# Optimization experiments

Measured on AMD Instinct MI355X. Metric: run time of the kernel, lower is better.

Reference implementation:

```python
import jax, jax.numpy as jnp
import numpy as np

CLIP = 50.0
EPS = 1e-8


def _attn_jacobian_agg(q, k, v, scale):
    """Aggregate attention Jacobian dO/dq summed over queries, plus attention outputs.

    q: (B, Q, d); k, v: (B, S, d).
    Per-query Jacobian: J_q = scale * sum_j p_j v_j (k_j - kbar)^T, kbar = sum_i p_i k_i.
    Returns (agg_jac: (B, d, d), outputs: (B, Q, d)).
    """
    scores = jnp.einsum('bqd,bsd->bqs', q, k) * scale
    p = jax.nn.softmax(scores, axis=-1)
    out = jnp.einsum('bqs,bsd->bqd', p, v)           # attention outputs O
    kbar = jnp.einsum('bqs,bsd->bqd', p, k)          # expected key per query
    # sum_j p_j v_j k_j^T  -> (B, Q, d, d)
    pvk = jnp.einsum('bqs,bsd,bse->bqde', p, v, k)
    jac = scale * (pvk - out[..., :, None] * kbar[..., None, :])
    return jac.sum(axis=1), out


def setup_inputs() -> dict:
    key = jax.random.key(0)
    ks = jax.random.split(key, 5)
    B, Q, S, M, D = 256, 16, 512, 8, 128
    return {
        'queries': jax.random.normal(ks[0], (B, Q, D), dtype=jnp.float32),
        'keys':    jax.random.normal(ks[1], (B, S, D), dtype=jnp.float32),
        'values':  jax.random.normal(ks[2], (B, S, D), dtype=jnp.float32),
        'k_cg':    jax.random.normal(ks[3], (B, M, D), dtype=jnp.float32),
        'v_cg':    jax.random.normal(ks[4], (B, M, D), dtype=jnp.float32),
    }


def reference(queries, keys, values, k_cg, v_cg):
    B, Q, d = queries.shape
    scale = d ** -0.5

    dense_jac, dense_out = _attn_jacobian_agg(queries, keys, values, scale)
    cg_jac, cg_out = _attn_jacobian_agg(queries, k_cg, v_cg, scale)

    # jacobian_clip_value = 50.0 (config default)
    dense_jac = jnp.clip(dense_jac, -CLIP, CLIP)
    cg_jac = jnp.clip(cg_jac, -CLIP, CLIP)

    df = dense_jac.reshape(B, -1)
    cf = cg_jac.reshape(B, -1)
    dn = jnp.linalg.norm(df, axis=-1)
    cn = jnp.linalg.norm(cf, axis=-1)
    cosine_sim = (df * cf).sum(axis=-1) / (dn * cn + EPS)
    force_direction_loss = 1.0 - cosine_sim

    # consistency: per-query output MSE, averaged over queries, scaled by 1/d_head
    out_diff = dense_out - cg_out
    per_query_mse = (out_diff ** 2).sum(axis=-1)          # (B, Q)
    consistency_loss = per_query_mse.sum(axis=-1) / Q / d  # (B,)

    # v4 loss: L = w_dir * L_force_cos + w_cons * L_consistency (defaults 1.0, 1.0)
    total = 1.0 * force_direction_loss + 1.0 * consistency_loss
    return total.mean()  # reduction='mean'
```

## Files before the change

### kernel.cpp

```cpp
#include <hip/hip_runtime.h>
#include <math.h>


namespace {
constexpr int Bn = 256, Qn = 16, Sn = 512, Mn = 8, Dn = 128;
constexpr int NT = 512;
constexpr float SCALE = 0.08838834764831845f;
constexpr float CLIPV = 50.0f;

constexpr int QS    = 0;
constexpr int PB    = 4352;
constexpr int WOFF  = 20992;
constexpr int ARENA = 23040;
constexpr int KT    = ARENA;
constexpr int VT    = ARENA + 18432;
constexpr int VTW   = ARENA + 27648;
constexpr int SCF   = ARENA;
constexpr int CGS   = 59904;
constexpr int PCG   = 60416;
constexpr int WC    = 61696;
constexpr int RED   = 61728;
constexpr int LDSZ  = 61856;

typedef __attribute__((ext_vector_type(8))) short bf16x8;
typedef __attribute__((ext_vector_type(4))) float f32x4;
#define MFMA16(a, b, c) __builtin_amdgcn_mfma_f32_16x16x32_bf16((a), (b), (c), 0, 0, 0)

__device__ inline unsigned int pack2t(float a, float b) {
  return __builtin_amdgcn_perm(__builtin_bit_cast(unsigned int, b),
                               __builtin_bit_cast(unsigned int, a), 0x07060302u);
}
__device__ inline unsigned short f2bf(float x) {
  unsigned int u = __builtin_bit_cast(unsigned int, x);
  u += 0x7fffu + ((u >> 16) & 1u);
  return (unsigned short)(u >> 16);
}
__device__ inline float bf2f(unsigned short h) {
  unsigned int u = ((unsigned int)h) << 16;
  return __builtin_bit_cast(float, u);
}
union Frag {
  bf16x8 v;
  unsigned int u[4];
  unsigned short h[8];
};

__global__ void zero_ws_kernel(float4* ws) {
  ws[threadIdx.x] = make_float4(0.f, 0.f, 0.f, 0.f);
}

__global__ void finalize_kernel(const float* __restrict__ ws, float* __restrict__ out) {
  __shared__ float sr[256];
  int i = threadIdx.x;
  float dt = ws[i * 4 + 0], n1 = ws[i * 4 + 1], n2 = ws[i * 4 + 2], cs = ws[i * 4 + 3];
  float cosv = dt / (sqrtf(n1) * sqrtf(n2) + 1e-8f);
  sr[i] = (1.0f - cosv) + cs * (1.0f / (float)(Qn * Dn));
  __syncthreads();
  for (int off = 128; off; off >>= 1) {
    if (i < off) sr[i] += sr[i + off];
    __syncthreads();
  }
  if (i == 0) out[0] = sr[0] * (1.0f / (float)Bn);
}

__global__ __launch_bounds__(NT, 4) void fm_kernel(
    const float* __restrict__ Qg, const float* __restrict__ Kg,
    const float* __restrict__ Vg, const float* __restrict__ Kcg,
    const float* __restrict__ Vcg, float* __restrict__ ws) {
  __shared__ __align__(16) char L[LDSZ];
  const int bid = blockIdx.x, b = bid >> 1, h = bid & 1;
  const int t = threadIdx.x, lane = t & 63, wv = t >> 6;
  const int quad = lane >> 4, l16 = lane & 15;

  const float* Qb = Qg + (size_t)b * Qn * Dn;
  const float* Kb = Kg + (size_t)b * Sn * Dn;
  const float* Vb = Vg + (size_t)b * Sn * Dn;
  const float* Kc = Kcg + (size_t)b * Mn * Dn;
  const float* Vc = Vcg + (size_t)b * Mn * Dn;

  const int dK = t & 127, gK = t >> 7;
  const int dV = t & 63, gV = t >> 6;
  float kpf[2][8], vpf[8];

  auto load_tiles = [&](int st) {
#pragma unroll
    for (int o = 0; o < 2; ++o) {
      int s0 = st * 64 + (gK + 4 * o) * 8;
#pragma unroll
      for (int i = 0; i < 8; ++i) kpf[o][i] = Kb[(size_t)(s0 + i) * Dn + dK];
    }
    int s1 = st * 64 + gV * 8;
#pragma unroll
    for (int i = 0; i < 8; ++i) vpf[i] = Vb[(size_t)(s1 + i) * Dn + h * 64 + dV];
  };
  auto store_tiles = [&](int st) {
#pragma unroll
    for (int o = 0; o < 2; ++o) {
      unsigned int u0 = pack2t(kpf[o][0], kpf[o][1]), u1 = pack2t(kpf[o][2], kpf[o][3]);
      unsigned int u2 = pack2t(kpf[o][4], kpf[o][5]), u3 = pack2t(kpf[o][6], kpf[o][7]);
      *(uint4*)(L + KT + dK * 144 + (gK + 4 * o) * 16) = make_uint4(u0, u1, u2, u3);
    }
    int s1 = st * 64 + gV * 8;
    float wv8[8];
#pragma unroll
    for (int i = 0; i < 8; ++i) wv8[i] = *(const float*)(L + WOFF + (s1 + i) * 4);
    unsigned int v0 = pack2t(vpf[0], vpf[1]), v1 = pack2t(vpf[2], vpf[3]);
    unsigned int v2 = pack2t(vpf[4], vpf[5]), v3 = pack2t(vpf[6], vpf[7]);
    *(uint4*)(L + VT + dV * 144 + gV * 16) = make_uint4(v0, v1, v2, v3);
    unsigned int w0 = pack2t(wv8[0] * vpf[0], wv8[1] * vpf[1]);
    unsigned int w1 = pack2t(wv8[2] * vpf[2], wv8[3] * vpf[3]);
    unsigned int w2 = pack2t(wv8[4] * vpf[4], wv8[5] * vpf[5]);
    unsigned int w3 = pack2t(wv8[6] * vpf[6], wv8[7] * vpf[7]);
    *(uint4*)(L + VTW + dV * 144 + gV * 16) = make_uint4(w0, w1, w2, w3);
  };

  {
    int row = t >> 5, c4 = t & 31;
    float4 qv = ((const float4*)Qb)[t];
    unsigned int p0 = pack2t(qv.x * SCALE, qv.y * SCALE);
    unsigned int p1 = pack2t(qv.z * SCALE, qv.w * SCALE);
    *(unsigned long long*)(L + QS + row * 272 + c4 * 8) =
        (unsigned long long)p0 | ((unsigned long long)p1 << 32);
  }
  load_tiles(0);
  __syncthreads();

  {
    bf16x8 aq[4];
#pragma unroll
    for (int kk = 0; kk < 4; ++kk)
      aq[kk] = *(const bf16x8*)(L + QS + l16 * 272 + kk * 64 + quad * 16);
    for (int j = 0; j < 4; ++j) {
      int srow = 64 * wv + 16 * j + l16;
      const float* kp = Kb + (size_t)srow * Dn + quad * 8;
      f32x4 acc = {0.f, 0.f, 0.f, 0.f};
#pragma unroll
      for (int kk = 0; kk < 4; ++kk) {
        float4 lo = *(const float4*)(kp + kk * 32);
        float4 hi = *(const float4*)(kp + kk * 32 + 4);
        Frag f;
        f.u[0] = pack2t(lo.x, lo.y);
        f.u[1] = pack2t(lo.z, lo.w);
        f.u[2] = pack2t(hi.x, hi.y);
        f.u[3] = pack2t(hi.z, hi.w);
        acc = MFMA16(aq[kk], f.v, acc);
      }
      int s = 64 * wv + 16 * j + l16;
#pragma unroll
      for (int r = 0; r < 4; ++r)
        *(float*)(L + SCF + (quad * 4 + r) * 2064 + s * 4) = acc[r];
    }
  }
  __syncthreads();

#pragma unroll
  for (int rr = 0; rr < 2; ++rr) {
    int q = wv * 2 + rr;
    const float* srow = (const float*)(L + SCF + q * 2064);
    float x[8];
    float m = -1e30f;
#pragma unroll
    for (int i = 0; i < 8; ++i) { x[i] = srow[lane * 8 + i]; m = fmaxf(m, x[i]); }
#pragma unroll
    for (int o = 32; o; o >>= 1) m = fmaxf(m, __shfl_xor(m, o));
    float ssum = 0.f;
#pragma unroll
    for (int i = 0; i < 8; ++i) { x[i] = __expf(x[i] - m); ssum += x[i]; }
#pragma unroll
    for (int o = 32; o; o >>= 1) ssum += __shfl_xor(ssum, o);
    float inv = 1.f / ssum;
    Frag g;
#pragma unroll
    for (int i = 0; i < 8; ++i) g.h[i] = f2bf(x[i] * inv);
    *(bf16x8*)(L + PB + q * 1040 + lane * 16) = g.v;
  }
  __syncthreads();
  {
    float wsv = 0.f;
#pragma unroll
    for (int q = 0; q < Qn; ++q)
      wsv += bf2f(*(const unsigned short*)(L + PB + q * 1040 + t * 2));
    *(float*)(L + WOFF + t * 4) = wsv;
  }
  __syncthreads();

  const int rp = wv & 1, ch = wv >> 1;
  f32x4 C00 = {0.f,0.f,0.f,0.f}, C01 = {0.f,0.f,0.f,0.f};
  f32x4 C10 = {0.f,0.f,0.f,0.f}, C11 = {0.f,0.f,0.f,0.f};
  f32x4 outacc = {0.f,0.f,0.f,0.f}, kbacc = {0.f,0.f,0.f,0.f};

  auto ckstep = [&](int colByte, f32x4& c00, f32x4& c01, f32x4& c10, f32x4& c11) {
    bf16x8 A0 = *(const bf16x8*)(L + VTW + (rp * 32 + l16) * 144 + colByte + quad * 16);
    bf16x8 A1 = *(const bf16x8*)(L + VTW + (rp * 32 + 16 + l16) * 144 + colByte + quad * 16);
    bf16x8 B0 = *(const bf16x8*)(L + KT + (ch * 32 + l16) * 144 + colByte + quad * 16);
    bf16x8 B1 = *(const bf16x8*)(L + KT + (ch * 32 + 16 + l16) * 144 + colByte + quad * 16);
    c00 = MFMA16(A0, B0, c00);
    c01 = MFMA16(A0, B1, c01);
    c10 = MFMA16(A1, B0, c10);
    c11 = MFMA16(A1, B1, c11);
  };

  for (int st = 0; st < 8; ++st) {
    if (st) __syncthreads();
    store_tiles(st);
    __syncthreads();
    if (st < 7) load_tiles(st + 1);
#pragma unroll
    for (int z = 0; z < 2; ++z) {
      int colByte = z * 64;
      bf16x8 pA = *(const bf16x8*)(L + PB + l16 * 1040 + st * 128 + z * 64 + quad * 16);
      bf16x8 bK = *(const bf16x8*)(L + KT + (wv * 16 + l16) * 144 + colByte + quad * 16);
      kbacc = MFMA16(pA, bK, kbacc);
      if (wv < 4) {
        bf16x8 bV = *(const bf16x8*)(L + VT + (wv * 16 + l16) * 144 + colByte + quad * 16);
        outacc = MFMA16(pA, bV, outacc);
      }
      ckstep(colByte, C00, C01, C10, C11);
    }
  }
  __syncthreads();

  if (wv < 4) {
#pragma unroll
    for (int r = 0; r < 4; ++r)
      *(unsigned short*)(L + VTW + (wv * 16 + l16) * 144 + (quad * 4 + r) * 2) = f2bf(-outacc[r]);
  }
#pragma unroll
  for (int r = 0; r < 4; ++r)
    *(unsigned short*)(L + KT + (wv * 16 + l16) * 144 + (quad * 4 + r) * 2) = f2bf(kbacc[r]);
  if (t < 256) {
    *(uint4*)(L + KT + (t >> 1) * 144 + 32 + (t & 1) * 16) = make_uint4(0, 0, 0, 0);
  } else if (t < 384) {
    int i = t - 256;
    *(uint4*)(L + VTW + (i >> 1) * 144 + 32 + (i & 1) * 16) = make_uint4(0, 0, 0, 0);
  }
  __syncthreads();
  ckstep(0, C00, C01, C10, C11);
#pragma unroll
  for (int r = 0; r < 4; ++r) {
    C00[r] = fminf(fmaxf(SCALE * C00[r], -CLIPV), CLIPV);
    C01[r] = fminf(fmaxf(SCALE * C01[r], -CLIPV), CLIPV);
    C10[r] = fminf(fmaxf(SCALE * C10[r], -CLIPV), CLIPV);
    C11[r] = fminf(fmaxf(SCALE * C11[r], -CLIPV), CLIPV);
  }
  __syncthreads();

  if (wv == 0) {
    f32x4 acc = {0.f, 0.f, 0.f, 0.f};
    const float* kp = Kc + (size_t)(l16 & 7) * Dn + quad * 8;
#pragma unroll
    for (int kk = 0; kk < 4; ++kk) {
      bf16x8 a = *(const bf16x8*)(L + QS + l16 * 272 + kk * 64 + quad * 16);
      float4 lo = *(const float4*)(kp + kk * 32);
      float4 hi = *(const float4*)(kp + kk * 32 + 4);
      Frag f;
      f.u[0] = pack2t(lo.x, lo.y);
      f.u[1] = pack2t(lo.z, lo.w);
      f.u[2] = pack2t(hi.x, hi.y);
      f.u[3] = pack2t(hi.z, hi.w);
      acc = MFMA16(a, f.v, acc);
    }
    if (l16 < 8) {
#pragma unroll
      for (int r = 0; r < 4; ++r)
        *(float*)(L + CGS + (quad * 4 + r) * 32 + l16 * 4) = acc[r];
    }
  }
  __syncthreads();
  if (t < 16) {
    float xs[8];
    float m = -1e30f;
#pragma unroll
    for (int s = 0; s < 8; ++s) { xs[s] = *(const float*)(L + CGS + t * 32 + s * 4); m = fmaxf(m, xs[s]); }
    float ssum = 0.f;
#pragma unroll
    for (int s = 0; s < 8; ++s) { xs[s] = __expf(xs[s] - m); ssum += xs[s]; }
    float inv = 1.f / ssum;
#pragma unroll
    for (int s = 0; s < 4; ++s)
      *(unsigned int*)(L + PCG + t * 80 + s * 4) = pack2t(xs[2 * s] * inv, xs[2 * s + 1] * inv);
#pragma unroll
    for (int p = 4; p < 16; ++p) *(unsigned int*)(L + PCG + t * 80 + p * 4) = 0u;
  }
  __syncthreads();
  if (t < 8) {
    float s = 0.f;
#pragma unroll
    for (int q = 0; q < Qn; ++q) s += bf2f(*(const unsigned short*)(L + PCG + q * 80 + t * 2));
    *(float*)(L + WC + t * 4) = s;
  }
  __syncthreads();
  if (t < 128) {
    float kv[8];
#pragma unroll
    for (int i = 0; i < 8; ++i) kv[i] = Kc[(size_t)i * Dn + t];
    *(uint4*)(L + KT + t * 144) = make_uint4(pack2t(kv[0], kv[1]), pack2t(kv[2], kv[3]),
                                             pack2t(kv[4], kv[5]), pack2t(kv[6], kv[7]));
    *(uint4*)(L + KT + t * 144 + 16) = make_uint4(0, 0, 0, 0);
    *(uint4*)(L + KT + t * 144 + 32) = make_uint4(0, 0, 0, 0);
    *(uint4*)(L + KT + t * 144 + 48) = make_uint4(0, 0, 0, 0);
  } else if (t < 192) {
    int d = t - 128;
    float vv2[8];
#pragma unroll
    for (int i = 0; i < 8; ++i) vv2[i] = Vc[(size_t)i * Dn + h * 64 + d];
    *(uint4*)(L + VT + d * 144) = make_uint4(pack2t(vv2[0], vv2[1]), pack2t(vv2[2], vv2[3]),
                                             pack2t(vv2[4], vv2[5]), pack2t(vv2[6], vv2[7]));
    *(uint4*)(L + VT + d * 144 + 16) = make_uint4(0, 0, 0, 0);
    *(uint4*)(L + VT + d * 144 + 32) = make_uint4(0, 0, 0, 0);
    *(uint4*)(L + VT + d * 144 + 48) = make_uint4(0, 0, 0, 0);
  } else if (t < 256) {
    int d = t - 192;
    float vv2[8], wcv[8];
#pragma unroll
    for (int i = 0; i < 8; ++i) {
      vv2[i] = Vc[(size_t)i * Dn + h * 64 + d];
      wcv[i] = *(const float*)(L + WC + i * 4);
    }
    *(uint4*)(L + VTW + d * 144) =
        make_uint4(pack2t(wcv[0] * vv2[0], wcv[1] * vv2[1]), pack2t(wcv[2] * vv2[2], wcv[3] * vv2[3]),
                   pack2t(wcv[4] * vv2[4], wcv[5] * vv2[5]), pack2t(wcv[6] * vv2[6], wcv[7] * vv2[7]));
    *(uint4*)(L + VTW + d * 144 + 16) = make_uint4(0, 0, 0, 0);
    *(uint4*)(L + VTW + d * 144 + 32) = make_uint4(0, 0, 0, 0);
    *(uint4*)(L + VTW + d * 144 + 48) = make_uint4(0, 0, 0, 0);
  }
  __syncthreads();
  f32x4 outc = {0.f,0.f,0.f,0.f}, kbc = {0.f,0.f,0.f,0.f};
  f32x4 D00 = {0.f,0.f,0.f,0.f}, D01 = {0.f,0.f,0.f,0.f};
  f32x4 D10 = {0.f,0.f,0.f,0.f}, D11 = {0.f,0.f,0.f,0.f};
  {
    bf16x8 pA = *(const bf16x8*)(L + PCG + l16 * 80 + quad * 16);
    bf16x8 bK = *(const bf16x8*)(L + KT + (wv * 16 + l16) * 144 + quad * 16);
    kbc = MFMA16(pA, bK, kbc);
    if (wv < 4) {
      bf16x8 bV = *(const bf16x8*)(L + VT + (wv * 16 + l16) * 144 + quad * 16);
      outc = MFMA16(pA, bV, outc);
    }
    ckstep(0, D00, D01, D10, D11);
  }
  __syncthreads();
  if (wv < 4) {
#pragma unroll
    for (int r = 0; r < 4; ++r)
      *(unsigned short*)(L + VTW + (wv * 16 + l16) * 144 + (quad * 4 + r) * 2) = f2bf(-outc[r]);
  }
#pragma unroll
  for (int r = 0; r < 4; ++r)
    *(unsigned short*)(L + KT + (wv * 16 + l16) * 144 + (quad * 4 + r) * 2) = f2bf(kbc[r]);
  __syncthreads();
  ckstep(0, D00, D01, D10, D11);
#pragma unroll
  for (int r = 0; r < 4; ++r) {
    D00[r] = fminf(fmaxf(SCALE * D00[r], -CLIPV), CLIPV);
    D01[r] = fminf(fmaxf(SCALE * D01[r], -CLIPV), CLIPV);
    D10[r] = fminf(fmaxf(SCALE * D10[r], -CLIPV), CLIPV);
    D11[r] = fminf(fmaxf(SCALE * D11[r], -CLIPV), CLIPV);
  }

  float dot = 0.f, nd2 = 0.f, nc2 = 0.f, cons = 0.f;
#pragma unroll
  for (int r = 0; r < 4; ++r) {
    dot += C00[r] * D00[r] + C01[r] * D01[r] + C10[r] * D10[r] + C11[r] * D11[r];
    nd2 += C00[r] * C00[r] + C01[r] * C01[r] + C10[r] * C10[r] + C11[r] * C11[r];
    nc2 += D00[r] * D00[r] + D01[r] * D01[r] + D10[r] * D10[r] + D11[r] * D11[r];
  }
  if (wv < 4) {
#pragma unroll
    for (int r = 0; r < 4; ++r) {
      float df = outacc[r] - outc[r];
      cons += df * df;
    }
  }
#pragma unroll
  for (int o = 32; o; o >>= 1) {
    dot += __shfl_xor(dot, o);
    nd2 += __shfl_xor(nd2, o);
    nc2 += __shfl_xor(nc2, o);
    cons += __shfl_xor(cons, o);
  }
  if (lane == 0) {
    float* red = (float*)(L + RED);
    red[wv * 4 + 0] = dot;
    red[wv * 4 + 1] = nd2;
    red[wv * 4 + 2] = nc2;
    red[wv * 4 + 3] = cons;
  }
  __syncthreads();
  if (t == 0) {
    const float* red = (const float*)(L + RED);
    float d_ = 0.f, n1 = 0.f, n2 = 0.f, cs = 0.f;
#pragma unroll
    for (int w = 0; w < 8; ++w) {
      d_ += red[w * 4 + 0];
      n1 += red[w * 4 + 1];
      n2 += red[w * 4 + 2];
      cs += red[w * 4 + 3];
    }
    atomicAdd(ws + b * 4 + 0, d_);
    atomicAdd(ws + b * 4 + 1, n1);
    atomicAdd(ws + b * 4 + 2, n2);
    atomicAdd(ws + b * 4 + 3, cs);
  }
}
}

extern "C" void kernel_launch(void* const* d_in, const int* in_sizes, int n_in,
                              void* d_out, int out_size, void* d_ws, size_t ws_size,
                              hipStream_t stream) {
  const float* q = (const float*)d_in[0];
  const float* k = (const float*)d_in[1];
  const float* v = (const float*)d_in[2];
  const float* kc = (const float*)d_in[3];
  const float* vc = (const float*)d_in[4];
  float* out = (float*)d_out;
  float* ws = (float*)d_ws;
  zero_ws_kernel<<<1, 256, 0, stream>>>((float4*)ws);
  fm_kernel<<<2 * Bn, NT, 0, stream>>>(q, k, v, kc, vc, ws);
  finalize_kernel<<<1, 256, 0, stream>>>(ws, out);
}
```

Measured before the change: 169.0 us.

## Split scores/softmax into separate per-batch kernel, removing duplicate work across halves

Before, each of the two blocks per batch recomputed the full Q·K scores, softmax and column weights. Now a separate scores_kernel does this once per batch, with register-resident softmax reductions, and writes probabilities, weights and the coarse-grained probabilities to the workspace. jac_kernel reads these back, and its block index is remapped so that both halves of a batch run close together for L2 reuse. The zero kernel is folded into scores_kernel. The cost is an extra launch and a global-memory round trip for the probability matrix, and K is read one more time.

```diff
diff --git a/kernel.cpp b/kernel.cpp
--- a/kernel.cpp
+++ b/kernel.cpp
@@ -8,19 +8,10 @@
 constexpr float SCALE = 0.08838834764831845f;
 constexpr float CLIPV = 50.0f;
 
-constexpr int QS    = 0;
-constexpr int PB    = 4352;
-constexpr int WOFF  = 20992;
-constexpr int ARENA = 23040;
-constexpr int KT    = ARENA;
-constexpr int VT    = ARENA + 18432;
-constexpr int VTW   = ARENA + 27648;
-constexpr int SCF   = ARENA;
-constexpr int CGS   = 59904;
-constexpr int PCG   = 60416;
-constexpr int WC    = 61696;
-constexpr int RED   = 61728;
-constexpr int LDSZ  = 61856;
+constexpr int W_OFF_F = 1048576;
+constexpr int PCG_OFF_B = 4718592;
+constexpr int WC_OFF_F = 1196032;
+constexpr int PART_OFF_F = 1198080;
 
 typedef __attribute__((ext_vector_type(8))) short bf16x8;
 typedef __attribute__((ext_vector_type(4))) float f32x4;
@@ -45,212 +36,43 @@
   unsigned short h[8];
 };
 
-__global__ void zero_ws_kernel(float4* ws) {
-  ws[threadIdx.x] = make_float4(0.f, 0.f, 0.f, 0.f);
-}
-
-__global__ void finalize_kernel(const float* __restrict__ ws, float* __restrict__ out) {
-  __shared__ float sr[256];
-  int i = threadIdx.x;
-  float dt = ws[i * 4 + 0], n1 = ws[i * 4 + 1], n2 = ws[i * 4 + 2], cs = ws[i * 4 + 3];
-  float cosv = dt / (sqrtf(n1) * sqrtf(n2) + 1e-8f);
-  sr[i] = (1.0f - cosv) + cs * (1.0f / (float)(Qn * Dn));
-  __syncthreads();
-  for (int off = 128; off; off >>= 1) {
-    if (i < off) sr[i] += sr[i + off];
-    __syncthreads();
-  }
-  if (i == 0) out[0] = sr[0] * (1.0f / (float)Bn);
-}
-
-__global__ __launch_bounds__(NT, 4) void fm_kernel(
+constexpr int A_QS = 0, A_PB = 4352, A_RDM = 20992, A_RDS = 21504,
+              A_CGS = 22016, A_CGP = 22528, A_LDSZ = 22784;
+
+__global__ __launch_bounds__(NT) void scores_kernel(
     const float* __restrict__ Qg, const float* __restrict__ Kg,
-    const float* __restrict__ Vg, const float* __restrict__ Kcg,
-    const float* __restrict__ Vcg, float* __restrict__ ws) {
-  __shared__ __align__(16) char L[LDSZ];
-  const int bid = blockIdx.x, b = bid >> 1, h = bid & 1;
-  const int t = threadIdx.x, lane = t & 63, wv = t >> 6;
-  const int quad = lane >> 4, l16 = lane & 15;
-
+    const float* __restrict__ Kcg, float* __restrict__ ws) {
+  __shared__ __align__(16) char L[A_LDSZ];
+  const int b = blockIdx.x, t = threadIdx.x;
+  const int lane = t & 63, wv = t >> 6, quad = lane >> 4, l16 = lane & 15;
   const float* Qb = Qg + (size_t)b * Qn * Dn;
   const float* Kb = Kg + (size_t)b * Sn * Dn;
-  const float* Vb = Vg + (size_t)b * Sn * Dn;
   const float* Kc = Kcg + (size_t)b * Mn * Dn;
-  const float* Vc = Vcg + (size_t)b * Mn * Dn;
-
-  const int dK = t & 127, gK = t >> 7;
-  const int dV = t & 63, gV = t >> 6;
-  float kpf[2][8], vpf[8];
-
-  auto load_tiles = [&](int st) {
-#pragma unroll
-    for (int o = 0; o < 2; ++o) {
-      int s0 = st * 64 + (gK + 4 * o) * 8;
-#pragma unroll
-      for (int i = 0; i < 8; ++i) kpf[o][i] = Kb[(size_t)(s0 + i) * Dn + dK];
-    }
-    int s1 = st * 64 + gV * 8;
-#pragma unroll
-    for (int i = 0; i < 8; ++i) vpf[i] = Vb[(size_t)(s1 + i) * Dn + h * 64 + dV];
-  };
-  auto store_tiles = [&](int st) {
-#pragma unroll
-    for (int o = 0; o < 2; ++o) {
-      unsigned int u0 = pack2t(kpf[o][0], kpf[o][1]), u1 = pack2t(kpf[o][2], kpf[o][3]);
-      unsigned int u2 = pack2t(kpf[o][4], kpf[o][5]), u3 = pack2t(kpf[o][6], kpf[o][7]);
-      *(uint4*)(L + KT + dK * 144 + (gK + 4 * o) * 16) = make_uint4(u0, u1, u2, u3);
-    }
-    int s1 = st * 64 + gV * 8;
-    float wv8[8];
-#pragma unroll
-    for (int i = 0; i < 8; ++i) wv8[i] = *(const float*)(L + WOFF + (s1 + i) * 4);
-    unsigned int v0 = pack2t(vpf[0], vpf[1]), v1 = pack2t(vpf[2], vpf[3]);
-    unsigned int v2 = pack2t(vpf[4], vpf[5]), v3 = pack2t(vpf[6], vpf[7]);
-    *(uint4*)(L + VT + dV * 144 + gV * 16) = make_uint4(v0, v1, v2, v3);
-    unsigned int w0 = pack2t(wv8[0] * vpf[0], wv8[1] * vpf[1]);
-    unsigned int w1 = pack2t(wv8[2] * vpf[2], wv8[3] * vpf[3]);
-    unsigned int w2 = pack2t(wv8[4] * vpf[4], wv8[5] * vpf[5]);
-    unsigned int w3 = pack2t(wv8[6] * vpf[6], wv8[7] * vpf[7]);
-    *(uint4*)(L + VTW + dV * 144 + gV * 16) = make_uint4(w0, w1, w2, w3);
-  };
+
+  if (t == 0)
+    *(float4*)(ws + PART_OFF_F + b * 4) = make_float4(0.f, 0.f, 0.f, 0.f);
 
   {
     int row = t >> 5, c4 = t & 31;
     float4 qv = ((const float4*)Qb)[t];
     unsigned int p0 = pack2t(qv.x * SCALE, qv.y * SCALE);
     unsigned int p1 = pack2t(qv.z * SCALE, qv.w * SCALE);
-    *(unsigned long long*)(L + QS + row * 272 + c4 * 8) =
+    *(unsigned long long*)(L + A_QS + row * 272 + c4 * 8) =
         (unsigned long long)p0 | ((unsigned long long)p1 << 32);
   }
-  load_tiles(0);
-  __syncthreads();
-
-  {
-    bf16x8 aq[4];
-#pragma unroll
-    for (int kk = 0; kk < 4; ++kk)
-      aq[kk] = *(const bf16x8*)(L + QS + l16 * 272 + kk * 64 + quad * 16);
-    for (int j = 0; j < 4; ++j) {
-      int srow = 64 * wv + 16 * j + l16;
-      const float* kp = Kb + (size_t)srow * Dn + quad * 8;
-      f32x4 acc = {0.f, 0.f, 0.f, 0.f};
-#pragma unroll
-      for (int kk = 0; kk < 4; ++kk) {
-        float4 lo = *(const float4*)(kp + kk * 32);
-        float4 hi = *(const float4*)(kp + kk * 32 + 4);
-        Frag f;
-        f.u[0] = pack2t(lo.x, lo.y);
-        f.u[1] = pack2t(lo.z, lo.w);
-        f.u[2] = pack2t(hi.x, hi.y);
-        f.u[3] = pack2t(hi.z, hi.w);
-        acc = MFMA16(aq[kk], f.v, acc);
-      }
-      int s = 64 * wv + 16 * j + l16;
-#pragma unroll
-      for (int r = 0; r < 4; ++r)
-        *(float*)(L + SCF + (quad * 4 + r) * 2064 + s * 4) = acc[r];
-    }
-  }
-  __syncthreads();
-
-#pragma unroll
-  for (int rr = 0; rr < 2; ++rr) {
-    int q = wv * 2 + rr;
-    const float* srow = (const float*)(L + SCF + q * 2064);
-    float x[8];
-    float m = -1e30f;
-#pragma unroll
-    for (int i = 0; i < 8; ++i) { x[i] = srow[lane * 8 + i]; m = fmaxf(m, x[i]); }
-#pragma unroll
-    for (int o = 32; o; o >>= 1) m = fmaxf(m, __shfl_xor(m, o));
-    float ssum = 0.f;
-#pragma unroll
-    for (int i = 0; i < 8; ++i) { x[i] = __expf(x[i] - m); ssum += x[i]; }
-#pragma unroll
-    for (int o = 32; o; o >>= 1) ssum += __shfl_xor(ssum, o);
-    float inv = 1.f / ssum;
-    Frag g;
-#pragma unroll
-    for (int i = 0; i < 8; ++i) g.h[i] = f2bf(x[i] * inv);
-    *(bf16x8*)(L + PB + q * 1040 + lane * 16) = g.v;
-  }
-  __syncthreads();
-  {
-    float wsv = 0.f;
-#pragma unroll
-    for (int q = 0; q < Qn; ++q)
-      wsv += bf2f(*(const unsigned short*)(L + PB + q * 1040 + t * 2));
-    *(float*)(L + WOFF + t * 4) = wsv;
-  }
-  __syncthreads();
-
-  const int rp = wv & 1, ch = wv >> 1;
-  f32x4 C00 = {0.f,0.f,0.f,0.f}, C01 = {0.f,0.f,0.f,0.f};
-  f32x4 C10 = {0.f,0.f,0.f,0.f}, C11 = {0.f,0.f,0.f,0.f};
-  f32x4 outacc = {0.f,0.f,0.f,0.f}, kbacc = {0.f,0.f,0.f,0.f};
-
-  auto ckstep = [&](int colByte, f32x4& c00, f32x4& c01, f32x4& c10, f32x4& c11) {
-    bf16x8 A0 = *(const bf16x8*)(L + VTW + (rp * 32 + l16) * 144 + colByte + quad * 16);
-    bf16x8 A1 = *(const bf16x8*)(L + VTW + (rp * 32 + 16 + l16) * 144 + colByte + quad * 16);
-    bf16x8 B0 = *(const bf16x8*)(L + KT + (ch * 32 + l16) * 144 + colByte + quad * 16);
-    bf16x8 B1 = *(const bf16x8*)(L + KT + (ch * 32 + 16 + l16) * 144 + colByte + quad * 16);
-    c00 = MFMA16(A0, B0, c00);
-    c01 = MFMA16(A0, B1, c01);
-    c10 = MFMA16(A1, B0, c10);
-    c11 = MFMA16(A1, B1, c11);
-  };
-
-  for (int st = 0; st < 8; ++st) {
-    if (st) __syncthreads();
-    store_tiles(st);
-    __syncthreads();
-    if (st < 7) load_tiles(st + 1);
-#pragma unroll
-    for (int z = 0; z < 2; ++z) {
-      int colByte = z * 64;
-      bf16x8 pA = *(const bf16x8*)(L + PB + l16 * 1040 + st * 128 + z * 64 + quad * 16);
-      bf16x8 bK = *(const bf16x8*)(L + KT + (wv * 16 + l16) * 144 + colByte + quad * 16);
-      kbacc = MFMA16(pA, bK, kbacc);
-      if (wv < 4) {
-        bf16x8 bV = *(const bf16x8*)(L + VT + (wv * 16 + l16) * 144 + colByte + quad * 16);
-        outacc = MFMA16(pA, bV, outacc);
-      }
-      ckstep(colByte, C00, C01, C10, C11);
-    }
-  }
-  __syncthreads();
-
-  if (wv < 4) {
-#pragma unroll
-    for (int r = 0; r < 4; ++r)
-      *(unsigned short*)(L + VTW + (wv * 16 + l16) * 144 + (quad * 4 + r) * 2) = f2bf(-outacc[r]);
-  }
-#pragma unroll
-  for (int r = 0; r < 4; ++r)
-    *(unsigned short*)(L + KT + (wv * 16 + l16) * 144 + (quad * 4 + r) * 2) = f2bf(kbacc[r]);
-  if (t < 256) {
-    *(uint4*)(L + KT + (t >> 1) * 144 + 32 + (t & 1) * 16) = make_uint4(0, 0, 0, 0);
-  } else if (t < 384) {
-    int i = t - 256;
-    *(uint4*)(L + VTW + (i >> 1) * 144 + 32 + (i & 1) * 16) = make_uint4(0, 0, 0, 0);
-  }
-  __syncthreads();
-  ckstep(0, C00, C01, C10, C11);
-#pragma unroll
-  for (int r = 0; r < 4; ++r) {
-    C00[r] = fminf(fmaxf(SCALE * C00[r], -CLIPV), CLIPV);
-    C01[r] = fminf(fmaxf(SCALE * C01[r], -CLIPV), CLIPV);
-    C10[r] = fminf(fmaxf(SCALE * C10[r], -CLIPV), CLIPV);
-    C11[r] = fminf(fmaxf(SCALE * C11[r], -CLIPV), CLIPV);
-  }
-  __syncthreads();
-
-  if (wv == 0) {
-    f32x4 acc = {0.f, 0.f, 0.f, 0.f};
-    const float* kp = Kc + (size_t)(l16 & 7) * Dn + quad * 8;
+  __syncthreads();
+
+  bf16x8 aq[4];
+#pragma unroll
+  for (int kk = 0; kk < 4; ++kk)
+    aq[kk] = *(const bf16x8*)(L + A_QS + l16 * 272 + kk * 64 + quad * 16);
+  f32x4 acc[4];
+#pragma unroll
+  for (int j = 0; j < 4; ++j) {
+    const float* kp = Kb + (size_t)(64 * wv + 16 * j + l16) * Dn + quad * 8;
+    f32x4 a = {0.f, 0.f, 0.f, 0.f};
 #pragma unroll
     for (int kk = 0; kk < 4; ++kk) {
-      bf16x8 a = *(const bf16x8*)(L + QS + l16 * 272 + kk * 64 + quad * 16);
       float4 lo = *(const float4*)(kp + kk * 32);
       float4 hi = *(const float4*)(kp + kk * 32 + 4);
       Frag f;
@@ -258,82 +80,307 @@
       f.u[1] = pack2t(lo.z, lo.w);
       f.u[2] = pack2t(hi.x, hi.y);
       f.u[3] = pack2t(hi.z, hi.w);
-      acc = MFMA16(a, f.v, acc);
-    }
-    if (l16 < 8) {
+      a = MFMA16(aq[kk], f.v, a);
+    }
+    acc[j] = a;
+  }
+  {
+    float pm[4];
+#pragma unroll
+    for (int r = 0; r < 4; ++r)
+      pm[r] = fmaxf(fmaxf(acc[0][r], acc[1][r]), fmaxf(acc[2][r], acc[3][r]));
+#pragma unroll
+    for (int o = 1; o < 16; o <<= 1)
+#pragma unroll
+      for (int r = 0; r < 4; ++r) pm[r] = fmaxf(pm[r], __shfl_xor(pm[r], o));
+    if (l16 == 0)
+#pragma unroll
+      for (int r = 0; r < 4; ++r) *(float*)(L + A_RDM + (quad * 4 + r) * 32 + wv * 4) = pm[r];
+  }
+  __syncthreads();
+  float gm[4];
+#pragma unroll
+  for (int r = 0; r < 4; ++r) {
+    const float* p = (const float*)(L + A_RDM + (quad * 4 + r) * 32);
+    float m = p[0];
+#pragma unroll
+    for (int w = 1; w < 8; ++w) m = fmaxf(m, p[w]);
+    gm[r] = m;
+  }
+  float e[4][4];
+  {
+    float ps[4] = {0.f, 0.f, 0.f, 0.f};
+#pragma unroll
+    for (int j = 0; j < 4; ++j)
+#pragma unroll
+      for (int r = 0; r < 4; ++r) {
+        e[j][r] = __expf(acc[j][r] - gm[r]);
+        ps[r] += e[j][r];
+      }
+#pragma unroll
+    for (int o = 1; o < 16; o <<= 1)
+#pragma unroll
+      for (int r = 0; r < 4; ++r) ps[r] += __shfl_xor(ps[r], o);
+    if (l16 == 0)
+#pragma unroll
+      for (int r = 0; r < 4; ++r) *(float*)(L + A_RDS + (quad * 4 + r) * 32 + wv * 4) = ps[r];
+  }
+  __syncthreads();
+  float inv[4];
+#pragma unroll
+  for (int r = 0; r < 4; ++r) {
+    const float* p = (const float*)(L + A_RDS + (quad * 4 + r) * 32);
+    float s = 0.f;
+#pragma unroll
+    for (int w = 0; w < 8; ++w) s += p[w];
+    inv[r] = 1.f / s;
+  }
+#pragma unroll
+  for (int j = 0; j < 4; ++j)
+#pragma unroll
+    for (int r = 0; r < 4; ++r)
+      *(unsigned short*)(L + A_PB + (quad * 4 + r) * 1040 + (64 * wv + 16 * j + l16) * 2) =
+          f2bf(e[j][r] * inv[r]);
+  __syncthreads();
+  {
+    float wsum = 0.f;
+#pragma unroll
+    for (int q = 0; q < Qn; ++q)
+      wsum += bf2f(*(const unsigned short*)(L + A_PB + q * 1040 + t * 2));
+    ws[W_OFF_F + b * 512 + t] = wsum;
+  }
+#pragma unroll
+  for (int i = 0; i < 2; ++i) {
+    int idx = t + i * 512, q = idx >> 6, c = idx & 63;
+    *(uint4*)((char*)ws + (size_t)b * 16384 + q * 1024 + c * 16) =
+        *(const uint4*)(L + A_PB + q * 1040 + c * 16);
+  }
+  if (wv == 0) {
+    const float* kp = Kc + (size_t)(l16 & 7) * Dn + quad * 8;
+    f32x4 a = {0.f, 0.f, 0.f, 0.f};
+#pragma unroll
+    for (int kk = 0; kk < 4; ++kk) {
+      float4 lo = *(const float4*)(kp + kk * 32);
+      float4 hi = *(const float4*)(kp + kk * 32 + 4);
+      Frag f;
+      f.u[0] = pack2t(lo.x, lo.y);
+      f.u[1] = pack2t(lo.z, lo.w);
+      f.u[2] = pack2t(hi.x, hi.y);
+      f.u[3] = pack2t(hi.z, hi.w);
+      a = MFMA16(aq[kk], f.v, a);
+    }
+    if (l16 < 8)
 #pragma unroll
       for (int r = 0; r < 4; ++r)
-        *(float*)(L + CGS + (quad * 4 + r) * 32 + l16 * 4) = acc[r];
-    }
+        *(float*)(L + A_CGS + (quad * 4 + r) * 32 + l16 * 4) = a[r];
   }
   __syncthreads();
   if (t < 16) {
     float xs[8];
     float m = -1e30f;
 #pragma unroll
-    for (int s = 0; s < 8; ++s) { xs[s] = *(const float*)(L + CGS + t * 32 + s * 4); m = fmaxf(m, xs[s]); }
+    for (int s = 0; s < 8; ++s) {
+      xs[s] = *(const float*)(L + A_CGS + t * 32 + s * 4);
+      m = fmaxf(m, xs[s]);
+    }
     float ssum = 0.f;
 #pragma unroll
-    for (int s = 0; s < 8; ++s) { xs[s] = __expf(xs[s] - m); ssum += xs[s]; }
-    float inv = 1.f / ssum;
-#pragma unroll
-    for (int s = 0; s < 4; ++s)
-      *(unsigned int*)(L + PCG + t * 80 + s * 4) = pack2t(xs[2 * s] * inv, xs[2 * s + 1] * inv);
-#pragma unroll
-    for (int p = 4; p < 16; ++p) *(unsigned int*)(L + PCG + t * 80 + p * 4) = 0u;
+    for (int s = 0; s < 8; ++s) {
+      xs[s] = __expf(xs[s] - m);
+      ssum += xs[s];
+    }
+    float iv = 1.f / ssum;
+    uint4 pk = make_uint4(pack2t(xs[0] * iv, xs[1] * iv), pack2t(xs[2] * iv, xs[3] * iv),
+                          pack2t(xs[4] * iv, xs[5] * iv), pack2t(xs[6] * iv, xs[7] * iv));
+    *(uint4*)(L + A_CGP + t * 16) = pk;
+    *(uint4*)((char*)ws + PCG_OFF_B + b * 256 + t * 16) = pk;
   }
   __syncthreads();
   if (t < 8) {
     float s = 0.f;
 #pragma unroll
-    for (int q = 0; q < Qn; ++q) s += bf2f(*(const unsigned short*)(L + PCG + q * 80 + t * 2));
-    *(float*)(L + WC + t * 4) = s;
-  }
-  __syncthreads();
+    for (int q = 0; q < Qn; ++q)
+      s += bf2f(*(const unsigned short*)(L + A_CGP + q * 16 + t * 2));
+    ws[WC_OFF_F + b * 8 + t] = s;
+  }
+}
+
+constexpr int B_PB = 0, B_WOFF = 16640, B_KT = 18688, B_VT = 37120, B_VTW = 46336,
+              B_PCG = 55552, B_WC = 56832, B_RED = 56864, B_LDSZ = 56992;
+
+__global__ __launch_bounds__(NT, 4) void jac_kernel(
+    const float* __restrict__ Kg, const float* __restrict__ Vg,
+    const float* __restrict__ Kcg, const float* __restrict__ Vcg,
+    float* __restrict__ ws) {
+  __shared__ __align__(16) char L[B_LDSZ];
+  const int g = blockIdx.x;
+  const int h = (g >> 3) & 1;
+  const int b = (g & 7) | ((g >> 4) << 3);
+  const int t = threadIdx.x, lane = t & 63, wv = t >> 6;
+  const int quad = lane >> 4, l16 = lane & 15;
+
+  const float* Kb = Kg + (size_t)b * Sn * Dn;
+  const float* Vb = Vg + (size_t)b * Sn * Dn;
+  const float* Kc = Kcg + (size_t)b * Mn * Dn;
+  const float* Vc = Vcg + (size_t)b * Mn * Dn;
+
+  const int dK = t & 127, gK = t >> 7;
+  const int dV = t & 63, gV = t >> 6;
+  float kpf[2][8], vpf[8];
+
+  auto load_tiles = [&](int st) {
+#pragma unroll
+    for (int o = 0; o < 2; ++o) {
+      int s0 = st * 64 + (gK + 4 * o) * 8;
+#pragma unroll
+      for (int i = 0; i < 8; ++i) kpf[o][i] = Kb[(size_t)(s0 + i) * Dn + dK];
+    }
+    int s1 = st * 64 + gV * 8;
+#pragma unroll
+    for (int i = 0; i < 8; ++i) vpf[i] = Vb[(size_t)(s1 + i) * Dn + h * 64 + dV];
+  };
+  auto store_tiles = [&](int st) {
+#pragma unroll
+    for (int o = 0; o < 2; ++o) {
+      unsigned int u0 = pack2t(kpf[o][0], kpf[o][1]), u1 = pack2t(kpf[o][2], kpf[o][3]);
+      unsigned int u2 = pack2t(kpf[o][4], kpf[o][5]), u3 = pack2t(kpf[o][6], kpf[o][7]);
+      *(uint4*)(L + B_KT + dK * 144 + (gK + 4 * o) * 16) = make_uint4(u0, u1, u2, u3);
+    }
+    int s1 = st * 64 + gV * 8;
+    float w8[8];
+#pragma unroll
+    for (int i = 0; i < 8; ++i) w8[i] = *(const float*)(L + B_WOFF + (s1 + i) * 4);
+    *(uint4*)(L + B_VT + dV * 144 + gV * 16) =
+        make_uint4(pack2t(vpf[0], vpf[1]), pack2t(vpf[2], vpf[3]),
+                   pack2t(vpf[4], vpf[5]), pack2t(vpf[6], vpf[7]));
+    *(uint4*)(L + B_VTW + dV * 144 + gV * 16) =
+        make_uint4(pack2t(w8[0] * vpf[0], w8[1] * vpf[1]), pack2t(w8[2] * vpf[2], w8[3] * vpf[3]),
+                   pack2t(w8[4] * vpf[4], w8[5] * vpf[5]), pack2t(w8[6] * vpf[6], w8[7] * vpf[7]));
+  };
+
+#pragma unroll
+  for (int i = 0; i < 2; ++i) {
+    int idx = t + i * 512, q = idx >> 6, c = idx & 63;
+    *(uint4*)(L + B_PB + q * 1040 + c * 16) =
+        *(const uint4*)((const char*)ws + (size_t)b * 16384 + q * 1024 + c * 16);
+  }
+  *(float*)(L + B_WOFF + t * 4) = ws[W_OFF_F + b * 512 + t];
+  if (t < 16) {
+    uint4 pv = *(const uint4*)((const char*)ws + PCG_OFF_B + b * 256 + t * 16);
+    *(uint4*)(L + B_PCG + t * 80) = pv;
+    *(uint4*)(L + B_PCG + t * 80 + 16) = make_uint4(0, 0, 0, 0);
+    *(uint4*)(L + B_PCG + t * 80 + 32) = make_uint4(0, 0, 0, 0);
+    *(uint4*)(L + B_PCG + t * 80 + 48) = make_uint4(0, 0, 0, 0);
+  }
+  if (t < 8) *(float*)(L + B_WC + t * 4) = ws[WC_OFF_F + b * 8 + t];
+  load_tiles(0);
+  __syncthreads();
+
+  const int rp = wv & 1, ch = wv >> 1;
+  f32x4 C00 = {0.f,0.f,0.f,0.f}, C01 = {0.f,0.f,0.f,0.f};
+  f32x4 C10 = {0.f,0.f,0.f,0.f}, C11 = {0.f,0.f,0.f,0.f};
+  f32x4 outacc = {0.f,0.f,0.f,0.f}, kbacc = {0.f,0.f,0.f,0.f};
+
+  auto ckstep = [&](int colByte, f32x4& c00, f32x4& c01, f32x4& c10, f32x4& c11) {
+    bf16x8 A0 = *(const bf16x8*)(L + B_VTW + (rp * 32 + l16) * 144 + colByte + quad * 16);
+    bf16x8 A1 = *(const bf16x8*)(L + B_VTW + (rp * 32 + 16 + l16) * 144 + colByte + quad * 16);
+    bf16x8 B0 = *(const bf16x8*)(L + B_KT + (ch * 32 + l16) * 144 + colByte + quad * 16);
+    bf16x8 B1 = *(const bf16x8*)(L + B_KT + (ch * 32 + 16 + l16) * 144 + colByte + quad * 16);
+    c00 = MFMA16(A0, B0, c00);
+    c01 = MFMA16(A0, B1, c01);
+    c10 = MFMA16(A1, B0, c10);
+    c11 = MFMA16(A1, B1, c11);
+  };
+
+  for (int st = 0; st < 8; ++st) {
+    if (st) __syncthreads();
+    store_tiles(st);
+    __syncthreads();
+    if (st < 7) load_tiles(st + 1);
+#pragma unroll
+    for (int z = 0; z < 2; ++z) {
+      int colByte = z * 64;
+      bf16x8 pA = *(const bf16x8*)(L + B_PB + l16 * 1040 + st * 128 + z * 64 + quad * 16);
+      bf16x8 bK = *(const bf16x8*)(L + B_KT + (wv * 16 + l16) * 144 + colByte + quad * 16);
+      kbacc = MFMA16(pA, bK, kbacc);
+      if (wv < 4) {
+        bf16x8 bV = *(const bf16x8*)(L + B_VT + (wv * 16 + l16) * 144 + colByte + quad * 16);
+        outacc = MFMA16(pA, bV, outacc);
+      }
+      ckstep(colByte, C00, C01, C10, C11);
+    }
+  }
+  __syncthreads();
+
+  if (wv < 4) {
+#pragma unroll
+    for (int r = 0; r < 4; ++r)
+      *(unsigned short*)(L + B_VTW + (wv * 16 + l16) * 144 + (quad * 4 + r) * 2) = f2bf(-outacc[r]);
+  }
+#pragma unroll
+  for (int r = 0; r < 4; ++r)
+    *(unsigned short*)(L + B_KT + (wv * 16 + l16) * 144 + (quad * 4 + r) * 2) = f2bf(kbacc[r]);
+  if (t < 256) {
+    *(uint4*)(L + B_KT + (t >> 1) * 144 + 32 + (t & 1) * 16) = make_uint4(0, 0, 0, 0);
+  } else if (t < 384) {
+    int i = t - 256;
+    *(uint4*)(L + B_VTW + (i >> 1) * 144 + 32 + (i & 1) * 16) = make_uint4(0, 0, 0, 0);
+  }
+  __syncthreads();
+  ckstep(0, C00, C01, C10, C11);
+#pragma unroll
+  for (int r = 0; r < 4; ++r) {
+    C00[r] = fminf(fmaxf(SCALE * C00[r], -CLIPV), CLIPV);
+    C01[r] = fminf(fmaxf(SCALE * C01[r], -CLIPV), CLIPV);
+    C10[r] = fminf(fmaxf(SCALE * C10[r], -CLIPV), CLIPV);
+    C11[r] = fminf(fmaxf(SCALE * C11[r], -CLIPV), CLIPV);
+  }
+  __syncthreads();
+
   if (t < 128) {
     float kv[8];
 #pragma unroll
     for (int i = 0; i < 8; ++i) kv[i] = Kc[(size_t)i * Dn + t];
-    *(uint4*)(L + KT + t * 144) = make_uint4(pack2t(kv[0], kv[1]), pack2t(kv[2], kv[3]),
-                                             pack2t(kv[4], kv[5]), pack2t(kv[6], kv[7]));
-    *(uint4*)(L + KT + t * 144 + 16) = make_uint4(0, 0, 0, 0);
-    *(uint4*)(L + KT + t * 144 + 32) = make_uint4(0, 0, 0, 0);
-    *(uint4*)(L + KT + t * 144 + 48) = make_uint4(0, 0, 0, 0);
+    *(uint4*)(L + B_KT + t * 144) = make_uint4(pack2t(kv[0], kv[1]), pack2t(kv[2], kv[3]),
+                                               pack2t(kv[4], kv[5]), pack2t(kv[6], kv[7]));
+    *(uint4*)(L + B_KT + t * 144 + 16) = make_uint4(0, 0, 0, 0);
+    *(uint4*)(L + B_KT + t * 144 + 32) = make_uint4(0, 0, 0, 0);
+    *(uint4*)(L + B_KT + t * 144 + 48) = make_uint4(0, 0, 0, 0);
   } else if (t < 192) {
     int d = t - 128;
-    float vv2[8];
-#pragma unroll
-    for (int i = 0; i < 8; ++i) vv2[i] = Vc[(size_t)i * Dn + h * 64 + d];
-    *(uint4*)(L + VT + d * 144) = make_uint4(pack2t(vv2[0], vv2[1]), pack2t(vv2[2], vv2[3]),
-                                             pack2t(vv2[4], vv2[5]), pack2t(vv2[6], vv2[7]));
-    *(uint4*)(L + VT + d * 144 + 16) = make_uint4(0, 0, 0, 0);
-    *(uint4*)(L + VT + d * 144 + 32) = make_uint4(0, 0, 0, 0);
-    *(uint4*)(L + VT + d * 144 + 48) = make_uint4(0, 0, 0, 0);
+    float v2[8];
+#pragma unroll
+    for (int i = 0; i < 8; ++i) v2[i] = Vc[(size_t)i * Dn + h * 64 + d];
+    *(uint4*)(L + B_VT + d * 144) = make_uint4(pack2t(v2[0], v2[1]), pack2t(v2[2], v2[3]),
+                                               pack2t(v2[4], v2[5]), pack2t(v2[6], v2[7]));
+    *(uint4*)(L + B_VT + d * 144 + 16) = make_uint4(0, 0, 0, 0);
+    *(uint4*)(L + B_VT + d * 144 + 32) = make_uint4(0, 0, 0, 0);
+    *(uint4*)(L + B_VT + d * 144 + 48) = make_uint4(0, 0, 0, 0);
   } else if (t < 256) {
     int d = t - 192;
-    float vv2[8], wcv[8];
+    float v2[8], wc[8];
 #pragma unroll
     for (int i = 0; i < 8; ++i) {
-      vv2[i] = Vc[(size_t)i * Dn + h * 64 + d];
-      wcv[i] = *(const float*)(L + WC + i * 4);
-    }
-    *(uint4*)(L + VTW + d * 144) =
-        make_uint4(pack2t(wcv[0] * vv2[0], wcv[1] * vv2[1]), pack2t(wcv[2] * vv2[2], wcv[3] * vv2[3]),
-                   pack2t(wcv[4] * vv2[4], wcv[5] * vv2[5]), pack2t(wcv[6] * vv2[6], wcv[7] * vv2[7]));
-    *(uint4*)(L + VTW + d * 144 + 16) = make_uint4(0, 0, 0, 0);
-    *(uint4*)(L + VTW + d * 144 + 32) = make_uint4(0, 0, 0, 0);
-    *(uint4*)(L + VTW + d * 144 + 48) = make_uint4(0, 0, 0, 0);
+      v2[i] = Vc[(size_t)i * Dn + h * 64 + d];
+      wc[i] = *(const float*)(L + B_WC + i * 4);
+    }
+    *(uint4*)(L + B_VTW + d * 144) =
+        make_uint4(pack2t(wc[0] * v2[0], wc[1] * v2[1]), pack2t(wc[2] * v2[2], wc[3] * v2[3]),
+                   pack2t(wc[4] * v2[4], wc[5] * v2[5]), pack2t(wc[6] * v2[6], wc[7] * v2[7]));
+    *(uint4*)(L + B_VTW + d * 144 + 16) = make_uint4(0, 0, 0, 0);
+    *(uint4*)(L + B_VTW + d * 144 + 32) = make_uint4(0, 0, 0, 0);
+    *(uint4*)(L + B_VTW + d * 144 + 48) = make_uint4(0, 0, 0, 0);
   }
   __syncthreads();
   f32x4 outc = {0.f,0.f,0.f,0.f}, kbc = {0.f,0.f,0.f,0.f};
   f32x4 D00 = {0.f,0.f,0.f,0.f}, D01 = {0.f,0.f,0.f,0.f};
   f32x4 D10 = {0.f,0.f,0.f,0.f}, D11 = {0.f,0.f,0.f,0.f};
   {
-    bf16x8 pA = *(const bf16x8*)(L + PCG + l16 * 80 + quad * 16);
-    bf16x8 bK = *(const bf16x8*)(L + KT + (wv * 16 + l16) * 144 + quad * 16);
+    bf16x8 pA = *(const bf16x8*)(L + B_PCG + l16 * 80 + quad * 16);
+    bf16x8 bK = *(const bf16x8*)(L + B_KT + (wv * 16 + l16) * 144 + quad * 16);
     kbc = MFMA16(pA, bK, kbc);
     if (wv < 4) {
-      bf16x8 bV = *(const bf16x8*)(L + VT + (wv * 16 + l16) * 144 + quad * 16);
+      bf16x8 bV = *(const bf16x8*)(L + B_VT + (wv * 16 + l16) * 144 + quad * 16);
       outc = MFMA16(pA, bV, outc);
     }
     ckstep(0, D00, D01, D10, D11);
@@ -342,11 +389,11 @@
   if (wv < 4) {
 #pragma unroll
     for (int r = 0; r < 4; ++r)
-      *(unsigned short*)(L + VTW + (wv * 16 + l16) * 144 + (quad * 4 + r) * 2) = f2bf(-outc[r]);
+      *(unsigned short*)(L + B_VTW + (wv * 16 + l16) * 144 + (quad * 4 + r) * 2) = f2bf(-outc[r]);
   }
 #pragma unroll
   for (int r = 0; r < 4; ++r)
-    *(unsigned short*)(L + KT + (wv * 16 + l16) * 144 + (quad * 4 + r) * 2) = f2bf(kbc[r]);
+    *(unsigned short*)(L + B_KT + (wv * 16 + l16) * 144 + (quad * 4 + r) * 2) = f2bf(kbc[r]);
   __syncthreads();
   ckstep(0, D00, D01, D10, D11);
 #pragma unroll
@@ -379,7 +426,7 @@
     cons += __shfl_xor(cons, o);
   }
   if (lane == 0) {
-    float* red = (float*)(L + RED);
+    float* red = (float*)(L + B_RED);
     red[wv * 4 + 0] = dot;
     red[wv * 4 + 1] = nd2;
     red[wv * 4 + 2] = nc2;
@@ -387,7 +434,7 @@
   }
   __syncthreads();
   if (t == 0) {
-    const float* red = (const float*)(L + RED);
+    const float* red = (const float*)(L + B_RED);
     float d_ = 0.f, n1 = 0.f, n2 = 0.f, cs = 0.f;
 #pragma unroll
     for (int w = 0; w < 8; ++w) {
@@ -396,11 +443,25 @@
       n2 += red[w * 4 + 2];
       cs += red[w * 4 + 3];
     }
-    atomicAdd(ws + b * 4 + 0, d_);
-    atomicAdd(ws + b * 4 + 1, n1);
-    atomicAdd(ws + b * 4 + 2, n2);
-    atomicAdd(ws + b * 4 + 3, cs);
-  }
+    atomicAdd(ws + PART_OFF_F + b * 4 + 0, d_);
+    atomicAdd(ws + PART_OFF_F + b * 4 + 1, n1);
+    atomicAdd(ws + PART_OFF_F + b * 4 + 2, n2);
+    atomicAdd(ws + PART_OFF_F + b * 4 + 3, cs);
+  }
+}
+
+__global__ void finalize_kernel(const float* __restrict__ ws, float* __restrict__ out) {
+  __shared__ float sr[256];
+  int i = threadIdx.x;
+  const float* p = ws + PART_OFF_F + i * 4;
+  float cosv = p[0] / (sqrtf(p[1]) * sqrtf(p[2]) + 1e-8f);
+  sr[i] = (1.0f - cosv) + p[3] * (1.0f / (float)(Qn * Dn));
+  __syncthreads();
+  for (int off = 128; off; off >>= 1) {
+    if (i < off) sr[i] += sr[i + off];
+    __syncthreads();
+  }
+  if (i == 0) out[0] = sr[0] * (1.0f / (float)Bn);
 }
 }
 
@@ -414,7 +475,7 @@
   const float* vc = (const float*)d_in[4];
   float* out = (float*)d_out;
   float* ws = (float*)d_ws;
-  zero_ws_kernel<<<1, 256, 0, stream>>>((float4*)ws);
-  fm_kernel<<<2 * Bn, NT, 0, stream>>>(q, k, v, kc, vc, ws);
+  scores_kernel<<<Bn, NT, 0, stream>>>(q, k, kc, ws);
+  jac_kernel<<<2 * Bn, NT, 0, stream>>>(k, v, kc, vc, ws);
   finalize_kernel<<<1, 256, 0, stream>>>(ws, out);
 }
```

New measurement: 171.7 us. No clear change (+1.6%).
